# Optimization experiments

Hardware: AMD Instinct MI355X
Metric: run time of the kernel (lower is better)

## Reference

```python
import jax, jax.numpy as jnp
import numpy as np

H, D = 4, 64  # num_heads, hidden_feats
IN_FEATS, OUT_FEATS = 1, 128
N_NODES, N_EDGES = 100000, 1600000
NEG_SLOPE = 0.2  # DGL GATConv default


def setup_inputs() -> dict:
    key = jax.random.key(0)
    ks = jax.random.split(key, 9)
    features = jax.random.normal(ks[0], (N_NODES, IN_FEATS), dtype=jnp.float32)
    src = jax.random.randint(ks[1], (N_EDGES,), 0, N_NODES)
    dst = jax.random.randint(ks[2], (N_EDGES,), 0, N_NODES)
    # GATConv params
    W = jax.random.normal(ks[3], (IN_FEATS, H * D), dtype=jnp.float32) * 0.5
    attn_l = jax.random.normal(ks[4], (H, D), dtype=jnp.float32) * 0.1
    attn_r = jax.random.normal(ks[5], (H, D), dtype=jnp.float32) * 0.1
    bias_gat = jnp.zeros((H * D,), dtype=jnp.float32)
    # fc params
    fc_W = jax.random.normal(ks[6], (H * D, OUT_FEATS), dtype=jnp.float32) * 0.05
    fc_b = jax.random.normal(ks[7], (OUT_FEATS,), dtype=jnp.float32) * 0.01
    return {"features": features, "W": W, "attn_l": attn_l, "attn_r": attn_r,
            "bias_gat": bias_gat, "fc_W": fc_W, "fc_b": fc_b,
            "src": src, "dst": dst}


def reference(features, W, attn_l, attn_r, bias_gat, fc_W, fc_b, src, dst):
    N = features.shape[0]
    # linear projection -> [N, H, D]
    feat = (features @ W).reshape(N, H, D)
    # per-node attention terms [N, H]
    el = jnp.einsum('nhd,hd->nh', feat, attn_l)
    er = jnp.einsum('nhd,hd->nh', feat, attn_r)
    # per-edge scores [E, H]
    e = jax.nn.leaky_relu(el[src] + er[dst], NEG_SLOPE)
    # segment softmax over incoming edges of each dst node
    emax = jax.ops.segment_max(e, dst, num_segments=N)  # [N, H]
    ee = jnp.exp(e - emax[dst])
    denom = jax.ops.segment_sum(ee, dst, num_segments=N)  # [N, H]
    alpha = ee / denom[dst]  # [E, H]
    # attention-weighted aggregation: scatter-add messages to dst
    msg = alpha[:, :, None] * feat[src]  # [E, H, D]
    rst = jax.ops.segment_sum(msg, dst, num_segments=N)  # [N, H, D]
    rst = rst + bias_gat.reshape(1, H, D)
    h = rst.reshape(N, H * D)
    out = h @ fc_W + fc_b  # [N, OUT_FEATS]
    return out.mean(axis=0)  # [OUT_FEATS]
```

## Files before the change

### kernel.cpp

```cpp
#include <hip/hip_runtime.h>

#define NEG_SLOPE 0.2f

#define GB_SHIFT 8
#define GB_NODES 256
#define GCAP 4864
#define NBLK 512
#define MAXB 512
#define SCHUNK 4096

#define DESC_OFF 1024
#define REC_OFF  (DESC_OFF + NBLK * MAXB * 4)


__global__ __launch_bounds__(512) void k_place(const int* __restrict__ src,
                                               const int* __restrict__ dst,
                                               int* __restrict__ desc,
                                               unsigned* __restrict__ rec,
                                               float* __restrict__ hdr,
                                               int E, int nbins, int chunk) {
    __shared__ unsigned       raw[SCHUNK];
    __shared__ unsigned short binb[SCHUNK];
    __shared__ unsigned       sorted[SCHUNK];
    __shared__ int hist[MAXB], startS[MAXB], cur[MAXB];
    __shared__ int wtot[8], wpre[8];

    int tid = threadIdx.x, blk = blockIdx.x;
    int lane = tid & 63, wave = tid >> 6;
    if (blk == 0 && tid < 16) hdr[tid] = 0.f;
    hist[tid] = 0;
    __syncthreads();

    int lo = blk * chunk;
    int hi = lo + chunk; if (hi > E) hi = E;
    int tot = hi - lo;

    for (int i = tid; i < tot; i += 512) {
        int d = dst[lo + i], s = src[lo + i];
        int b = d >> GB_SHIFT;
        raw[i]  = ((unsigned)(d & (GB_NODES - 1)) << 17) | (unsigned)s;
        binb[i] = (unsigned short)b;
        atomicAdd(&hist[b], 1);
    }
    __syncthreads();

    int h = hist[tid];
    int x = h;
    #pragma unroll
    for (int off = 1; off < 64; off <<= 1) {
        int y = __shfl_up(x, off, 64);
        if (lane >= off) x += y;
    }
    if (lane == 63) wtot[wave] = x;
    __syncthreads();
    if (tid < 8) {
        int t = wtot[tid];
        #pragma unroll
        for (int off = 1; off < 8; off <<= 1) {
            int y = __shfl_up(t, off, 64);
            if (tid >= off) t += y;
        }
        wpre[tid] = t - wtot[tid];
    }
    __syncthreads();
    int ex = (x - h) + wpre[wave];
    startS[tid] = ex;
    cur[tid] = ex;
    __syncthreads();

    for (int i = tid; i < tot; i += 512) {
        int p = atomicAdd(&cur[binb[i]], 1);
        sorted[p] = raw[i];
    }
    __syncthreads();

    size_t base = (size_t)blk * SCHUNK;
    for (int i = tid; i < tot; i += 512)
        rec[base + i] = sorted[i];
    desc[(size_t)blk * MAXB + tid] = (startS[tid] << 16) | hist[tid];
}

__global__ __launch_bounds__(512) void k_gather(const float* __restrict__ f,
                                                const float* __restrict__ W,
                                                const float* __restrict__ attn_l,
                                                const float* __restrict__ attn_r,
                                                const int* __restrict__ desc,
                                                const unsigned* __restrict__ rec,
                                                float* __restrict__ S_sum,
                                                int N) {
    __shared__ float    par[8];
    __shared__ int      deg[GB_NODES], nstart[GB_NODES], ncur[GB_NODES];
    __shared__ unsigned stageu[GCAP];
    __shared__ float    sortedf[GCAP];
    __shared__ int      wtot[8], wpre[8], cntS;
    __shared__ float    sm[8][4];

    int tid = threadIdx.x, lane = tid & 63, wave = tid >> 6;
    int bin = blockIdx.x, nbase = bin << GB_SHIFT;

    if (tid < 256) {
        float w  = W[tid];
        float vl = w * attn_l[tid];
        float vr = w * attn_r[tid];
        #pragma unroll
        for (int off = 32; off > 0; off >>= 1) {
            vl += __shfl_down(vl, off, 64);
            vr += __shfl_down(vr, off, 64);
        }
        if ((tid & 63) == 0) {
            int hh = tid >> 6;
            par[hh]     = vl;
            par[4 + hh] = vr;
        }
        deg[tid] = 0;
    }

    int dsc  = desc[(size_t)tid * MAXB + bin];
    int sst  = dsc >> 16, scnt = dsc & 0xFFFF;

    int x = scnt;
    #pragma unroll
    for (int off = 1; off < 64; off <<= 1) {
        int y = __shfl_up(x, off, 64);
        if (lane >= off) x += y;
    }
    if (lane == 63) wtot[wave] = x;
    __syncthreads();
    if (tid < 8) {
        int t = wtot[tid];
        #pragma unroll
        for (int off = 1; off < 8; off <<= 1) {
            int y = __shfl_up(t, off, 64);
            if (tid >= off) t += y;
        }
        wpre[tid] = t - wtot[tid];
        if (tid == 7) cntS = t;
    }
    __syncthreads();
    int soff = (x - scnt) + wpre[wave];

    float al[4], ar[4];
    #pragma unroll
    for (int h = 0; h < 4; ++h) { al[h] = par[h]; ar[h] = par[4 + h]; }

    {
        const unsigned* r0 = rec + (size_t)tid * SCHUNK + sst;
        for (int i = 0; i < scnt; ++i) {
            unsigned rc = r0[i];
            int p = soff + i;
            if (p < GCAP) {
                stageu[p] = rc;
                atomicAdd(&deg[rc >> 17], 1);
            }
        }
    }
    __syncthreads();
    int cnt = cntS; if (cnt > GCAP) cnt = GCAP;

    if (tid < GB_NODES) {
        int dv = deg[tid];
        int x2 = dv;
        #pragma unroll
        for (int off = 1; off < 64; off <<= 1) {
            int y = __shfl_up(x2, off, 64);
            if (lane >= off) x2 += y;
        }
        if (lane == 63) wtot[wave] = x2;
        __syncthreads();
        if (tid < 4) {
            int t = wtot[tid];
            #pragma unroll
            for (int off = 1; off < 4; off <<= 1) {
                int y = __shfl_up(t, off, 64);
                if (tid >= off) t += y;
            }
            wpre[tid] = t - wtot[tid];
        }
        __syncthreads();
        int ex = (x2 - dv) + wpre[wave];
        nstart[tid] = ex;
        ncur[tid]   = ex;
    } else {
        __syncthreads();
        __syncthreads();
    }
    __syncthreads();

    for (int i = tid; i < cnt; i += 512) {
        unsigned rc = stageu[i];
        int p = atomicAdd(&ncur[rc >> 17], 1);
        if (p < GCAP) sortedf[p] = f[rc & 0x1FFFF];
    }
    __syncthreads();

    int l   = tid >> 1, prt = tid & 1;
    int st  = nstart[l];
    int len = deg[l];
    int en  = st + len; if (en > GCAP) en = GCAP; if (st > GCAP) st = GCAP;
    float fd = (len > 0) ? f[nbase + l] : 0.f;

    float dn[4] = {0.f, 0.f, 0.f, 0.f};
    float nm[4] = {0.f, 0.f, 0.f, 0.f};
    float br[4];
    #pragma unroll
    for (int h = 0; h < 4; ++h) br[h] = fd * ar[h];
    for (int i = st + prt; i < en; i += 2) {
        float fs = sortedf[i];
        #pragma unroll
        for (int h = 0; h < 4; ++h) {
            float xx = fmaf(fs, al[h], br[h]);
            xx = (xx > 0.f) ? xx : NEG_SLOPE * xx;
            float ee = __expf(xx);
            dn[h] += ee;
            nm[h] += ee * fs;
        }
    }
    float v[4];
    #pragma unroll
    for (int h = 0; h < 4; ++h) {
        dn[h] += __shfl_xor(dn[h], 1, 64);
        nm[h] += __shfl_xor(nm[h], 1, 64);
        v[h] = (prt == 0 && dn[h] > 0.f) ? nm[h] / dn[h] : 0.f;
    }

    #pragma unroll
    for (int off = 32; off > 0; off >>= 1) {
        #pragma unroll
        for (int h = 0; h < 4; ++h) v[h] += __shfl_down(v[h], off, 64);
    }
    if (lane == 0) {
        #pragma unroll
        for (int h = 0; h < 4; ++h) sm[wave][h] = v[h];
    }
    __syncthreads();
    if (tid < 4) {
        float s = 0.f;
        #pragma unroll
        for (int w = 0; w < 8; ++w) s += sm[w][tid];
        atomicAdd(&S_sum[tid], s);
    }
}


__global__ void k_prep(const float* __restrict__ W,
                       const float* __restrict__ attn_l,
                       const float* __restrict__ attn_r,
                       float* __restrict__ ws) {
    int tid = threadIdx.x;
    float w  = W[tid];
    float vl = w * attn_l[tid];
    float vr = w * attn_r[tid];
    #pragma unroll
    for (int off = 32; off > 0; off >>= 1) {
        vl += __shfl_down(vl, off, 64);
        vr += __shfl_down(vr, off, 64);
    }
    if ((tid & 63) == 0) {
        int h = tid >> 6;
        ws[h]     = vl;
        ws[4 + h] = vr;
    }
}

__global__ void k_edge(const float* __restrict__ f,
                       const int* __restrict__ src,
                       const int* __restrict__ dst,
                       const float* __restrict__ par,
                       float* __restrict__ denom,
                       float* __restrict__ numer,
                       int E) {
    float al[4], ar[4];
    #pragma unroll
    for (int h = 0; h < 4; ++h) { al[h] = par[h]; ar[h] = par[4 + h]; }
    int stride = gridDim.x * blockDim.x;
    for (int e = blockIdx.x * blockDim.x + threadIdx.x; e < E; e += stride) {
        int s = src[e], d = dst[e];
        float fs = f[s], fd = f[d];
        #pragma unroll
        for (int h = 0; h < 4; ++h) {
            float x = fs * al[h] + fd * ar[h];
            x = (x > 0.f) ? x : NEG_SLOPE * x;
            float ee = __expf(x);
            atomicAdd(&denom[d * 4 + h], ee);
            atomicAdd(&numer[d * 4 + h], ee * fs);
        }
    }
}

__global__ void k_node(const float* __restrict__ denom,
                       const float* __restrict__ numer,
                       float* __restrict__ S_sum,
                       int N) {
    float acc[4] = {0.f, 0.f, 0.f, 0.f};
    int stride = gridDim.x * blockDim.x;
    for (int n = blockIdx.x * blockDim.x + threadIdx.x; n < N; n += stride) {
        float4 dn = *reinterpret_cast<const float4*>(&denom[(size_t)n * 4]);
        float4 nm = *reinterpret_cast<const float4*>(&numer[(size_t)n * 4]);
        acc[0] += (dn.x > 0.f) ? nm.x / dn.x : 0.f;
        acc[1] += (dn.y > 0.f) ? nm.y / dn.y : 0.f;
        acc[2] += (dn.z > 0.f) ? nm.z / dn.z : 0.f;
        acc[3] += (dn.w > 0.f) ? nm.w / dn.w : 0.f;
    }
    #pragma unroll
    for (int off = 32; off > 0; off >>= 1) {
        #pragma unroll
        for (int h = 0; h < 4; ++h) acc[h] += __shfl_down(acc[h], off, 64);
    }
    __shared__ float sm[4][4];
    int lane = threadIdx.x & 63;
    int wave = threadIdx.x >> 6;
    if (lane == 0) {
        #pragma unroll
        for (int h = 0; h < 4; ++h) sm[wave][h] = acc[h];
    }
    __syncthreads();
    if (threadIdx.x < 4) {
        float v = sm[0][threadIdx.x] + sm[1][threadIdx.x]
                + sm[2][threadIdx.x] + sm[3][threadIdx.x];
        atomicAdd(&S_sum[threadIdx.x], v);
    }
}

__global__ __launch_bounds__(512) void k_final(const float* __restrict__ ws,
                                               const float* __restrict__ W,
                                               const float* __restrict__ bias_gat,
                                               const float* __restrict__ fc_W,
                                               const float* __restrict__ fc_b,
                                               float* __restrict__ out,
                                               float invN) {
    __shared__ float sm[4][128];
    int tid = threadIdx.x;
    int o = tid & 127, part = tid >> 7;
    float sp = ws[8 + part] * invN;
    float acc = 0.f;
    #pragma unroll 4
    for (int k = 0; k < 64; ++k) {
        int hd = part * 64 + k;
        float rm = sp * W[hd] + bias_gat[hd];
        acc += rm * fc_W[hd * 128 + o];
    }
    sm[part][o] = acc;
    __syncthreads();
    if (tid < 128)
        out[tid] = sm[0][tid] + sm[1][tid] + sm[2][tid] + sm[3][tid] + fc_b[tid];
}

extern "C" void kernel_launch(void* const* d_in, const int* in_sizes, int n_in,
                              void* d_out, int out_size, void* d_ws, size_t ws_size,
                              hipStream_t stream) {
    const float* features = (const float*)d_in[0];
    const float* W        = (const float*)d_in[1];
    const float* attn_l   = (const float*)d_in[2];
    const float* attn_r   = (const float*)d_in[3];
    const float* bias_gat = (const float*)d_in[4];
    const float* fc_W     = (const float*)d_in[5];
    const float* fc_b     = (const float*)d_in[6];
    const int*   src      = (const int*)d_in[7];
    const int*   dst      = (const int*)d_in[8];
    int N = in_sizes[0];
    int E = in_sizes[7];

    float* ws = (float*)d_ws;
    int nbins = (N + GB_NODES - 1) >> GB_SHIFT;
    int chunk = (E + NBLK - 1) / NBLK;
    size_t need = (size_t)REC_OFF + (size_t)NBLK * SCHUNK * sizeof(unsigned);

    if (nbins <= MAXB && N <= (1 << 17) && chunk <= SCHUNK && ws_size >= need) {
        int* desc     = (int*)((char*)d_ws + DESC_OFF);
        unsigned* rec = (unsigned*)((char*)d_ws + REC_OFF);

        hipLaunchKernelGGL(k_place, dim3(NBLK), dim3(512), 0, stream,
                           src, dst, desc, rec, ws, E, nbins, chunk);
        hipLaunchKernelGGL(k_gather, dim3(nbins), dim3(512), 0, stream,
                           features, W, attn_l, attn_r, desc, rec, ws + 8, N);
    } else {
        float* denom = ws + 16;
        float* numer = denom + (size_t)N * 4;
        size_t zero_bytes = (16 + 2 * (size_t)N * 4) * sizeof(float);
        hipMemsetAsync(d_ws, 0, zero_bytes, stream);
        hipLaunchKernelGGL(k_prep, dim3(1), dim3(256), 0, stream, W, attn_l, attn_r, ws);
        int eb = (E + 255) / 256;
        hipLaunchKernelGGL(k_edge, dim3(eb), dim3(256), 0, stream,
                           features, src, dst, ws, denom, numer, E);
        int nb = (N + 255) / 256;
        if (nb > 2048) nb = 2048;
        hipLaunchKernelGGL(k_node, dim3(nb), dim3(256), 0, stream, denom, numer, ws + 8, N);
    }

    hipLaunchKernelGGL(k_final, dim3(1), dim3(512), 0, stream,
                       ws, W, bias_gat, fc_W, fc_b, (float*)d_out, 1.0f / (float)N);
}
```

Measured before the change: 45.79 us.

## Replace per-bin counting sort with direct LDS atomic accumulation per node

```diff
diff --git a/kernel.cpp b/kernel.cpp
--- a/kernel.cpp
+++ b/kernel.cpp
@@ -4,7 +4,6 @@
 
 #define GB_SHIFT 8
 #define GB_NODES 256
-#define GCAP 4864
 #define NBLK 512
 #define MAXB 512
 #define SCHUNK 4096
@@ -88,12 +87,10 @@
                                                 const unsigned* __restrict__ rec,
                                                 float* __restrict__ S_sum,
                                                 int N) {
-    __shared__ float    par[8];
-    __shared__ int      deg[GB_NODES], nstart[GB_NODES], ncur[GB_NODES];
-    __shared__ unsigned stageu[GCAP];
-    __shared__ float    sortedf[GCAP];
-    __shared__ int      wtot[8], wpre[8], cntS;
-    __shared__ float    sm[8][4];
+    __shared__ float par[8];
+    __shared__ float fl[GB_NODES];
+    __shared__ float acc[GB_NODES * 9];
+    __shared__ float sm[8][4];
 
     int tid = threadIdx.x, lane = tid & 63, wave = tid >> 6;
     int bin = blockIdx.x, nbase = bin << GB_SHIFT;
@@ -112,32 +109,13 @@
             par[hh]     = vl;
             par[4 + hh] = vr;
         }
-        deg[tid] = 0;
-    }
+        fl[tid] = (nbase + tid < N) ? f[nbase + tid] : 0.f;
+    }
+    for (int i = tid; i < GB_NODES * 9; i += 512) acc[i] = 0.f;
 
     int dsc  = desc[(size_t)tid * MAXB + bin];
     int sst  = dsc >> 16, scnt = dsc & 0xFFFF;
-
-    int x = scnt;
-    #pragma unroll
-    for (int off = 1; off < 64; off <<= 1) {
-        int y = __shfl_up(x, off, 64);
-        if (lane >= off) x += y;
-    }
-    if (lane == 63) wtot[wave] = x;
-    __syncthreads();
-    if (tid < 8) {
-        int t = wtot[tid];
-        #pragma unroll
-        for (int off = 1; off < 8; off <<= 1) {
-            int y = __shfl_up(t, off, 64);
-            if (tid >= off) t += y;
-        }
-        wpre[tid] = t - wtot[tid];
-        if (tid == 7) cntS = t;
-    }
-    __syncthreads();
-    int soff = (x - scnt) + wpre[wave];
+    __syncthreads();
 
     float al[4], ar[4];
     #pragma unroll
@@ -147,82 +125,31 @@
         const unsigned* r0 = rec + (size_t)tid * SCHUNK + sst;
         for (int i = 0; i < scnt; ++i) {
             unsigned rc = r0[i];
-            int p = soff + i;
-            if (p < GCAP) {
-                stageu[p] = rc;
-                atomicAdd(&deg[rc >> 17], 1);
+            int l = rc >> 17;
+            float fs = f[rc & 0x1FFFF];
+            float fd = fl[l];
+            float* a = &acc[l * 9];
+            #pragma unroll
+            for (int h = 0; h < 4; ++h) {
+                float xx = fmaf(fs, al[h], fd * ar[h]);
+                xx = (xx > 0.f) ? xx : NEG_SLOPE * xx;
+                float ee = __expf(xx);
+                atomicAdd(&a[h], ee);
+                atomicAdd(&a[4 + h], ee * fs);
             }
         }
     }
     __syncthreads();
-    int cnt = cntS; if (cnt > GCAP) cnt = GCAP;
-
+
+    float v[4] = {0.f, 0.f, 0.f, 0.f};
     if (tid < GB_NODES) {
-        int dv = deg[tid];
-        int x2 = dv;
-        #pragma unroll
-        for (int off = 1; off < 64; off <<= 1) {
-            int y = __shfl_up(x2, off, 64);
-            if (lane >= off) x2 += y;
-        }
-        if (lane == 63) wtot[wave] = x2;
-        __syncthreads();
-        if (tid < 4) {
-            int t = wtot[tid];
-            #pragma unroll
-            for (int off = 1; off < 4; off <<= 1) {
-                int y = __shfl_up(t, off, 64);
-                if (tid >= off) t += y;
-            }
-            wpre[tid] = t - wtot[tid];
-        }
-        __syncthreads();
-        int ex = (x2 - dv) + wpre[wave];
-        nstart[tid] = ex;
-        ncur[tid]   = ex;
-    } else {
-        __syncthreads();
-        __syncthreads();
-    }
-    __syncthreads();
-
-    for (int i = tid; i < cnt; i += 512) {
-        unsigned rc = stageu[i];
-        int p = atomicAdd(&ncur[rc >> 17], 1);
-        if (p < GCAP) sortedf[p] = f[rc & 0x1FFFF];
-    }
-    __syncthreads();
-
-    int l   = tid >> 1, prt = tid & 1;
-    int st  = nstart[l];
-    int len = deg[l];
-    int en  = st + len; if (en > GCAP) en = GCAP; if (st > GCAP) st = GCAP;
-    float fd = (len > 0) ? f[nbase + l] : 0.f;
-
-    float dn[4] = {0.f, 0.f, 0.f, 0.f};
-    float nm[4] = {0.f, 0.f, 0.f, 0.f};
-    float br[4];
-    #pragma unroll
-    for (int h = 0; h < 4; ++h) br[h] = fd * ar[h];
-    for (int i = st + prt; i < en; i += 2) {
-        float fs = sortedf[i];
+        const float* a = &acc[tid * 9];
         #pragma unroll
         for (int h = 0; h < 4; ++h) {
-            float xx = fmaf(fs, al[h], br[h]);
-            xx = (xx > 0.f) ? xx : NEG_SLOPE * xx;
-            float ee = __expf(xx);
-            dn[h] += ee;
-            nm[h] += ee * fs;
-        }
-    }
-    float v[4];
-    #pragma unroll
-    for (int h = 0; h < 4; ++h) {
-        dn[h] += __shfl_xor(dn[h], 1, 64);
-        nm[h] += __shfl_xor(nm[h], 1, 64);
-        v[h] = (prt == 0 && dn[h] > 0.f) ? nm[h] / dn[h] : 0.f;
-    }
-
+            float dn = a[h];
+            v[h] = (dn > 0.f) ? a[4 + h] / dn : 0.f;
+        }
+    }
     #pragma unroll
     for (int off = 32; off > 0; off >>= 1) {
         #pragma unroll
```

Result: slower. 116.2 us (+153.8%).

## Double gather block width and drop LDS staging buffers in place kernel

Applied to the files above, without the earlier changes.

```diff
diff --git a/kernel.cpp b/kernel.cpp
--- a/kernel.cpp
+++ b/kernel.cpp
@@ -19,9 +19,7 @@
                                                unsigned* __restrict__ rec,
                                                float* __restrict__ hdr,
                                                int E, int nbins, int chunk) {
-    __shared__ unsigned       raw[SCHUNK];
-    __shared__ unsigned short binb[SCHUNK];
-    __shared__ unsigned       sorted[SCHUNK];
+    __shared__ unsigned sorted[SCHUNK];
     __shared__ int hist[MAXB], startS[MAXB], cur[MAXB];
     __shared__ int wtot[8], wpre[8];
 
@@ -35,13 +33,8 @@
     int hi = lo + chunk; if (hi > E) hi = E;
     int tot = hi - lo;
 
-    for (int i = tid; i < tot; i += 512) {
-        int d = dst[lo + i], s = src[lo + i];
-        int b = d >> GB_SHIFT;
-        raw[i]  = ((unsigned)(d & (GB_NODES - 1)) << 17) | (unsigned)s;
-        binb[i] = (unsigned short)b;
-        atomicAdd(&hist[b], 1);
-    }
+    for (int i = tid; i < tot; i += 512)
+        atomicAdd(&hist[dst[lo + i] >> GB_SHIFT], 1);
     __syncthreads();
 
     int h = hist[tid];
@@ -69,8 +62,9 @@
     __syncthreads();
 
     for (int i = tid; i < tot; i += 512) {
-        int p = atomicAdd(&cur[binb[i]], 1);
-        sorted[p] = raw[i];
+        int d = dst[lo + i], s = src[lo + i];
+        int p = atomicAdd(&cur[d >> GB_SHIFT], 1);
+        sorted[p] = ((unsigned)(d & (GB_NODES - 1)) << 17) | (unsigned)s;
     }
     __syncthreads();
 
@@ -80,20 +74,21 @@
     desc[(size_t)blk * MAXB + tid] = (startS[tid] << 16) | hist[tid];
 }
 
-__global__ __launch_bounds__(512) void k_gather(const float* __restrict__ f,
-                                                const float* __restrict__ W,
-                                                const float* __restrict__ attn_l,
-                                                const float* __restrict__ attn_r,
-                                                const int* __restrict__ desc,
-                                                const unsigned* __restrict__ rec,
-                                                float* __restrict__ S_sum,
-                                                int N) {
+__global__ __launch_bounds__(1024) void k_gather(const float* __restrict__ f,
+                                                 const float* __restrict__ W,
+                                                 const float* __restrict__ attn_l,
+                                                 const float* __restrict__ attn_r,
+                                                 const int* __restrict__ desc,
+                                                 const unsigned* __restrict__ rec,
+                                                 float* __restrict__ S_sum,
+                                                 int N) {
     __shared__ float    par[8];
     __shared__ int      deg[GB_NODES], nstart[GB_NODES], ncur[GB_NODES];
+    __shared__ int      soffA[NBLK];
     __shared__ unsigned stageu[GCAP];
     __shared__ float    sortedf[GCAP];
     __shared__ int      wtot[8], wpre[8], cntS;
-    __shared__ float    sm[8][4];
+    __shared__ float    sm[16][4];
 
     int tid = threadIdx.x, lane = tid & 63, wave = tid >> 6;
     int bin = blockIdx.x, nbase = bin << GB_SHIFT;
@@ -115,16 +110,17 @@
         deg[tid] = 0;
     }
 
-    int dsc  = desc[(size_t)tid * MAXB + bin];
-    int sst  = dsc >> 16, scnt = dsc & 0xFFFF;
-
-    int x = scnt;
-    #pragma unroll
-    for (int off = 1; off < 64; off <<= 1) {
-        int y = __shfl_up(x, off, 64);
-        if (lane >= off) x += y;
-    }
-    if (lane == 63) wtot[wave] = x;
+    int sc = 0, x = 0;
+    if (tid < NBLK) {
+        sc = desc[(size_t)tid * MAXB + bin] & 0xFFFF;
+        x = sc;
+        #pragma unroll
+        for (int off = 1; off < 64; off <<= 1) {
+            int y = __shfl_up(x, off, 64);
+            if (lane >= off) x += y;
+        }
+        if (lane == 63) wtot[wave] = x;
+    }
     __syncthreads();
     if (tid < 8) {
         int t = wtot[tid];
@@ -137,15 +133,20 @@
         if (tid == 7) cntS = t;
     }
     __syncthreads();
-    int soff = (x - scnt) + wpre[wave];
+    if (tid < NBLK) soffA[tid] = (x - sc) + wpre[wave];
+    __syncthreads();
 
     float al[4], ar[4];
     #pragma unroll
     for (int h = 0; h < 4; ++h) { al[h] = par[h]; ar[h] = par[4 + h]; }
 
+    int seg = tid >> 1, half = tid & 1;
     {
-        const unsigned* r0 = rec + (size_t)tid * SCHUNK + sst;
-        for (int i = 0; i < scnt; ++i) {
+        int dsc  = desc[(size_t)seg * MAXB + bin];
+        int sst  = dsc >> 16, scnt = dsc & 0xFFFF;
+        int soff = soffA[seg];
+        const unsigned* r0 = rec + (size_t)seg * SCHUNK + sst;
+        for (int i = half; i < scnt; i += 2) {
             unsigned rc = r0[i];
             int p = soff + i;
             if (p < GCAP) {
@@ -157,43 +158,42 @@
     __syncthreads();
     int cnt = cntS; if (cnt > GCAP) cnt = GCAP;
 
+    int dv = 0, x2 = 0;
     if (tid < GB_NODES) {
-        int dv = deg[tid];
-        int x2 = dv;
+        dv = deg[tid]; x2 = dv;
         #pragma unroll
         for (int off = 1; off < 64; off <<= 1) {
             int y = __shfl_up(x2, off, 64);
             if (lane >= off) x2 += y;
         }
         if (lane == 63) wtot[wave] = x2;
-        __syncthreads();
-        if (tid < 4) {
-            int t = wtot[tid];
-            #pragma unroll
-            for (int off = 1; off < 4; off <<= 1) {
-                int y = __shfl_up(t, off, 64);
-                if (tid >= off) t += y;
-            }
-            wpre[tid] = t - wtot[tid];
-        }
-        __syncthreads();
-        int ex = (x2 - dv) + wpre[wave];
-        nstart[tid] = ex;
-        ncur[tid]   = ex;
-    } else {
-        __syncthreads();
-        __syncthreads();
-    }
-    __syncthreads();
-
-    for (int i = tid; i < cnt; i += 512) {
+    }
+    __syncthreads();
+    if (tid < 4) {
+        int t = wtot[tid];
+        #pragma unroll
+        for (int off = 1; off < 4; off <<= 1) {
+            int y = __shfl_up(t, off, 64);
+            if (tid >= off) t += y;
+        }
+        wpre[tid] = t - wtot[tid];
+    }
+    __syncthreads();
+    if (tid < GB_NODES) {
+        int ex2 = (x2 - dv) + wpre[wave];
+        nstart[tid] = ex2;
+        ncur[tid]   = ex2;
+    }
+    __syncthreads();
+
+    for (int i = tid; i < cnt; i += 1024) {
         unsigned rc = stageu[i];
         int p = atomicAdd(&ncur[rc >> 17], 1);
         if (p < GCAP) sortedf[p] = f[rc & 0x1FFFF];
     }
     __syncthreads();
 
-    int l   = tid >> 1, prt = tid & 1;
+    int l   = tid >> 2, prt = tid & 3;
     int st  = nstart[l];
     int len = deg[l];
     int en  = st + len; if (en > GCAP) en = GCAP; if (st > GCAP) st = GCAP;
@@ -204,7 +204,7 @@
     float br[4];
     #pragma unroll
     for (int h = 0; h < 4; ++h) br[h] = fd * ar[h];
-    for (int i = st + prt; i < en; i += 2) {
+    for (int i = st + prt; i < en; i += 4) {
         float fs = sortedf[i];
         #pragma unroll
         for (int h = 0; h < 4; ++h) {
@@ -220,6 +220,8 @@
     for (int h = 0; h < 4; ++h) {
         dn[h] += __shfl_xor(dn[h], 1, 64);
         nm[h] += __shfl_xor(nm[h], 1, 64);
+        dn[h] += __shfl_xor(dn[h], 2, 64);
+        nm[h] += __shfl_xor(nm[h], 2, 64);
         v[h] = (prt == 0 && dn[h] > 0.f) ? nm[h] / dn[h] : 0.f;
     }
 
@@ -236,7 +238,7 @@
     if (tid < 4) {
         float s = 0.f;
         #pragma unroll
-        for (int w = 0; w < 8; ++w) s += sm[w][tid];
+        for (int w = 0; w < 16; ++w) s += sm[w][tid];
         atomicAdd(&S_sum[tid], s);
     }
 }
@@ -371,7 +373,7 @@
 
         hipLaunchKernelGGL(k_place, dim3(NBLK), dim3(512), 0, stream,
                            src, dst, desc, rec, ws, E, nbins, chunk);
-        hipLaunchKernelGGL(k_gather, dim3(nbins), dim3(512), 0, stream,
+        hipLaunchKernelGGL(k_gather, dim3(nbins), dim3(1024), 0, stream,
                            features, W, attn_l, attn_r, desc, rec, ws + 8, N);
     } else {
         float* denom = ws + 16;
```

Result: faster. 43.93 us, median of 2 (-4.1%).
